# Kernel optimization log

Hardware: AMD Instinct MI355X
Metric: run time of the kernel (lower is better)

## Reference

```python
import jax, jax.numpy as jnp
import numpy as np

B, SX, SY, D = 32, 2048, 2048, 160

def setup_inputs() -> dict:
    key = jax.random.key(0)
    ks = jax.random.split(key, 5)
    s = 1.0 / np.sqrt(D)
    return {
        "x": jax.random.normal(ks[0], (B, SX, D), dtype=jnp.float32),
        "y": jax.random.normal(ks[1], (B, SY, D), dtype=jnp.float32),
        "Wq": jax.random.normal(ks[2], (D, D), dtype=jnp.float32) * s,
        "bq": jnp.zeros((D,), dtype=jnp.float32),
        "Wk": jax.random.normal(ks[3], (D, D), dtype=jnp.float32) * s,
        "bk": jnp.zeros((D,), dtype=jnp.float32),
        "Wv": jax.random.normal(ks[4], (D, D), dtype=jnp.float32) * s,
        "bv": jnp.zeros((D,), dtype=jnp.float32),
    }

def reference(x, y, Wq, bq, Wk, bk, Wv, bv):
    # torch nn.Linear: out = in @ W.T + b, W is [out_dim, in_dim]
    q = jnp.einsum('bxd,ed->bxe', x, Wq) + bq          # [B,SX,D]
    k = jnp.einsum('byd,ed->bye', y, Wk) + bk          # [B,SY,D]
    v = jnp.einsum('byd,ed->bye', y, Wv) + bv          # [B,SY,D]
    scores = jnp.einsum('bxd,byd->bxy', q, k)          # [B,SX,SY] (no scaling in source)
    attn = jax.nn.softmax(scores, axis=-1)
    out = jnp.einsum('bxy,byd->bxd', attn, v)          # dropout is identity at eval
    return out + x                                     # residual
```

## Files before the change

kernel.cpp:

```cpp
#include <hip/hip_runtime.h>

#define LOG2E 1.44269504088896340736f

typedef _Float16 f16;
typedef __attribute__((ext_vector_type(4))) _Float16 f16x4;
typedef __attribute__((ext_vector_type(8))) _Float16 f16x8;
typedef __attribute__((ext_vector_type(4))) float f32x4;
typedef __attribute__((ext_vector_type(8))) unsigned short us8;

#define BB 32
#define SSX 2048
#define SSY 2048
#define DD 160
#define M_TOTAL (BB*SSX)

#define PRS 168
#define VTRS 136
#define RS 168
#define P_RS 72

__device__ __forceinline__ f32x4 mfma16(f16x8 a, f16x8 b, f32x4 c) {
  return __builtin_amdgcn_mfma_f32_16x16x32_f16(a, b, c, 0, 0, 0);
}

__global__ __launch_bounds__(256, 2) void proj_kernel(
    const float* __restrict__ x, const float* __restrict__ y,
    const float* __restrict__ Wq, const float* __restrict__ bq,
    const float* __restrict__ Wk, const float* __restrict__ bk,
    const float* __restrict__ Wv, const float* __restrict__ bv,
    f16* __restrict__ Qw, f16* __restrict__ Kw, f16* __restrict__ Vtw)
{
  __shared__ __align__(16) f16 buf[160*PRS];
  const int t = threadIdx.x;
  const int wave = t >> 6;
  const int lane = t & 63;
  const int quad = lane >> 4;
  const int l16  = lane & 15;
  const int bid  = blockIdx.x;
  const int kind = bid % 3;
  const int tile = bid / 3;
  const int row0 = tile * 128;
  const float* src  = (kind == 0) ? x  : y;
  const float* W    = (kind == 0) ? Wq : (kind == 1 ? Wk : Wv);
  const float* bias = (kind == 0) ? bq : (kind == 1 ? bk : bv);

  for (int i = 0; i < 20; ++i) {
    int idx = t + i*256;
    int r = idx / 40, c4 = idx % 40;
    float4 v = *(const float4*)&src[(size_t)(row0 + r)*DD + c4*4];
    f16x4 h = { (f16)v.x, (f16)v.y, (f16)v.z, (f16)v.w };
    *(f16x4*)&buf[r*PRS + c4*4] = h;
  }
  __syncthreads();
  f16x8 afr0[5], afr1[5];
  #pragma unroll
  for (int ks = 0; ks < 5; ++ks) {
    afr0[ks] = *(const f16x8*)&buf[(wave*32 + l16)*PRS + ks*32 + quad*8];
    afr1[ks] = *(const f16x8*)&buf[(wave*32 + 16 + l16)*PRS + ks*32 + quad*8];
  }
  __syncthreads();

  for (int i = 0; i < 25; ++i) {
    int idx = t + i*256;
    int r = idx / 40, c4 = idx % 40;
    float4 v = *(const float4*)&W[r*160 + c4*4];
    f16x4 h = { (f16)v.x, (f16)v.y, (f16)v.z, (f16)v.w };
    *(f16x4*)&buf[r*PRS + c4*4] = h;
  }
  __syncthreads();

  f32x4 acc0[10], acc1[10];
  #pragma unroll
  for (int nt = 0; nt < 10; ++nt) {
    float bs = bias[nt*16 + l16];
    acc0[nt] = (f32x4){bs,bs,bs,bs};
    acc1[nt] = (f32x4){bs,bs,bs,bs};
    #pragma unroll
    for (int ks = 0; ks < 5; ++ks) {
      f16x8 bfr = *(const f16x8*)&buf[(nt*16 + l16)*PRS + ks*32 + quad*8];
      acc0[nt] = mfma16(afr0[ks], bfr, acc0[nt]);
      acc1[nt] = mfma16(afr1[ks], bfr, acc1[nt]);
    }
  }
  __syncthreads();

  if (kind < 2) {
    f16* dst = (kind == 0) ? Qw : Kw;
    #pragma unroll
    for (int nt = 0; nt < 10; ++nt)
      #pragma unroll
      for (int r = 0; r < 4; ++r) {
        buf[(wave*32 + quad*4 + r)*PRS + nt*16 + l16]      = (f16)acc0[nt][r];
        buf[(wave*32 + 16 + quad*4 + r)*PRS + nt*16 + l16] = (f16)acc1[nt][r];
      }
    __syncthreads();
    for (int i = 0; i < 10; ++i) {
      int idx = t + i*256;
      int r = idx / 20, g = idx % 20;
      *(us8*)&dst[(size_t)(row0 + r)*DD + g*8] = *(const us8*)&buf[r*PRS + g*8];
    }
  } else {
    #pragma unroll
    for (int nt = 0; nt < 10; ++nt)
      #pragma unroll
      for (int r = 0; r < 4; ++r) {
        buf[(nt*16 + l16)*VTRS + wave*32 + quad*4 + r]      = (f16)acc0[nt][r];
        buf[(nt*16 + l16)*VTRS + wave*32 + 16 + quad*4 + r] = (f16)acc1[nt][r];
      }
    __syncthreads();
    const int b  = row0 / SSY;
    const int y0 = row0 % SSY;
    for (int i = 0; i < 10; ++i) {
      int idx = t + i*256;
      int d = idx / 16, yg = idx % 16;
      *(us8*)&Vtw[((size_t)b*DD + d)*SSY + y0 + yg*8] = *(const us8*)&buf[d*VTRS + yg*8];
    }
  }
}


#define LOAD_CHUNK(yb) { \
  const f16* ksrc = Kw + ((size_t)b*SSY + (yb))*DD; \
  const f16* vsrc = Vtw + (size_t)b*DD*SSY + (yb); \
  _Pragma("unroll") \
  for (int i = 0; i < 5; ++i) { \
    int idx = t + i*256; int r = idx/20, c = idx%20; \
    kreg[i] = *(const us8*)&ksrc[(size_t)r*DD + c*8]; \
  } \
  _Pragma("unroll") \
  for (int i = 0; i < 5; ++i) { \
    int idx = t + i*256; int d = idx>>3, g = idx&7; \
    vreg[i] = *(const us8*)&vsrc[(size_t)d*SSY + g*8]; \
  } \
}

#define STORE_CHUNK() { \
  _Pragma("unroll") \
  for (int i = 0; i < 5; ++i) { \
    int idx = t + i*256; int r = idx/20, c = idx%20; \
    *(us8*)&K_lds[r*RS + c*8] = kreg[i]; \
  } \
  _Pragma("unroll") \
  for (int i = 0; i < 5; ++i) { \
    int idx = t + i*256; int d = idx>>3, g = idx&7; \
    *(us8*)&Vt_lds[d*64 + ((g ^ (d & 7)) << 3)] = vreg[i]; \
  } \
}

__global__ __launch_bounds__(256, 2) void flash_kernel(
    const f16* __restrict__ Qw, const f16* __restrict__ Kw, const f16* __restrict__ Vtw,
    const float* __restrict__ x, float* __restrict__ out)
{
  __shared__ __align__(16) f16 K_lds[64*RS];
  __shared__ __align__(16) f16 Vt_lds[176*64];
  __shared__ __align__(16) f16 P_lds[4*32*P_RS];
  const int t = threadIdx.x;
  const int wave = t >> 6;
  const int lane = t & 63;
  const int quad = lane >> 4;
  const int l16  = lane & 15;
  const int bid  = blockIdx.x;
  const int b    = bid >> 4;
  const int x0   = (bid & 15) * 128;

  for (int idx = t; idx < 1024; idx += 256) {
    int d = idx >> 6, yy = idx & 63;
    Vt_lds[(160 + d)*64 + yy] = (d == 0) ? (f16)1.0f : (f16)0.0f;
  }

  f16x8 qfr0[5], qfr1[5];
  #pragma unroll
  for (int h = 0; h < 2; ++h) {
    if (h) __syncthreads();
    const f16* qsrc = Qw + ((size_t)b*SSX + x0 + h*64)*DD;
    for (int i = 0; i < 5; ++i) {
      int idx = t + i*256;
      int r = idx / 20, c = idx % 20;
      *(us8*)&K_lds[r*RS + c*8] = *(const us8*)&qsrc[(size_t)r*DD + c*8];
    }
    __syncthreads();
    if ((wave >> 1) == h) {
      const int base = (wave & 1)*32;
      #pragma unroll
      for (int ks = 0; ks < 5; ++ks) {
        qfr0[ks] = *(const f16x8*)&K_lds[(base + l16)*RS + ks*32 + quad*8];
        qfr1[ks] = *(const f16x8*)&K_lds[(base + 16 + l16)*RS + ks*32 + quad*8];
      }
    }
  }

  f32x4 acc0[11], acc1[11];
  #pragma unroll
  for (int i = 0; i < 11; ++i) { acc0[i] = (f32x4){0.f,0.f,0.f,0.f}; acc1[i] = (f32x4){0.f,0.f,0.f,0.f}; }
  float m0[4], m1[4];
  #pragma unroll
  for (int r = 0; r < 4; ++r) { m0[r] = -1e30f; m1[r] = -1e30f; }

  f16* Pw = &P_lds[wave*32*P_RS];
  us8 kreg[5], vreg[5];

  LOAD_CHUNK(0);
  for (int yc = 0; yc < SSY/64; ++yc) {
    __syncthreads();
    STORE_CHUNK();
    __syncthreads();
    if (yc < SSY/64 - 1) LOAD_CHUNK((yc+1)*64);

    f32x4 S0[4], S1[4];
    #pragma unroll
    for (int nt = 0; nt < 4; ++nt) { S0[nt] = (f32x4){0.f,0.f,0.f,0.f}; S1[nt] = (f32x4){0.f,0.f,0.f,0.f}; }
    #pragma unroll
    for (int nt = 0; nt < 4; ++nt)
      #pragma unroll
      for (int ks = 0; ks < 5; ++ks) {
        f16x8 kfr = *(const f16x8*)&K_lds[(nt*16 + l16)*RS + ks*32 + quad*8];
        S0[nt] = mfma16(qfr0[ks], kfr, S0[nt]);
        S1[nt] = mfma16(qfr1[ks], kfr, S1[nt]);
      }

    float n0[4], n1[4];
    bool changed = false;
    #pragma unroll
    for (int r = 0; r < 4; ++r) {
      float a = fmaxf(fmaxf(S0[0][r], S0[1][r]), fmaxf(S0[2][r], S0[3][r]));
      #pragma unroll
      for (int off = 1; off < 16; off <<= 1) a = fmaxf(a, __shfl_xor(a, off));
      n0[r] = fmaxf(m0[r], a);
      changed = changed || (n0[r] > m0[r]);
      float c = fmaxf(fmaxf(S1[0][r], S1[1][r]), fmaxf(S1[2][r], S1[3][r]));
      #pragma unroll
      for (int off = 1; off < 16; off <<= 1) c = fmaxf(c, __shfl_xor(c, off));
      n1[r] = fmaxf(m1[r], c);
      changed = changed || (n1[r] > m1[r]);
    }
    if (__any(changed)) {
      f32x4 av0, av1;
      #pragma unroll
      for (int r = 0; r < 4; ++r) {
        av0[r] = exp2f((m0[r] - n0[r])*LOG2E); m0[r] = n0[r];
        av1[r] = exp2f((m1[r] - n1[r])*LOG2E); m1[r] = n1[r];
      }
      #pragma unroll
      for (int i = 0; i < 11; ++i) { acc0[i] *= av0; acc1[i] *= av1; }
    }

    #pragma unroll
    for (int r = 0; r < 4; ++r)
      #pragma unroll
      for (int nt = 0; nt < 4; ++nt) {
        Pw[(quad*4 + r)*P_RS + nt*16 + l16]      = (f16)exp2f((S0[nt][r] - m0[r])*LOG2E);
        Pw[(16 + quad*4 + r)*P_RS + nt*16 + l16] = (f16)exp2f((S1[nt][r] - m1[r])*LOG2E);
      }

    #pragma unroll
    for (int k2 = 0; k2 < 2; ++k2) {
      f16x8 p0 = *(const f16x8*)&Pw[l16*P_RS + k2*32 + quad*8];
      f16x8 p1 = *(const f16x8*)&Pw[(16 + l16)*P_RS + k2*32 + quad*8];
      #pragma unroll
      for (int dt = 0; dt < 11; ++dt) {
        f16x8 vfr = *(const f16x8*)&Vt_lds[(dt*16 + l16)*64 + (((k2*4 + quad) ^ (l16 & 7)) << 3)];
        acc0[dt] = mfma16(p0, vfr, acc0[dt]);
        acc1[dt] = mfma16(p1, vfr, acc1[dt]);
      }
    }
  }

  float rl0[4], rl1[4];
  #pragma unroll
  for (int r = 0; r < 4; ++r) {
    rl0[r] = 1.f / __shfl(acc0[10][r], lane & 48);
    rl1[r] = 1.f / __shfl(acc1[10][r], lane & 48);
  }
  const size_t base = ((size_t)b*SSX + x0 + wave*32)*DD;
  #pragma unroll
  for (int dt = 0; dt < 10; ++dt)
    #pragma unroll
    for (int r = 0; r < 4; ++r) {
      size_t o0 = base + (size_t)(quad*4 + r)*DD + dt*16 + l16;
      size_t o1 = base + (size_t)(16 + quad*4 + r)*DD + dt*16 + l16;
      out[o0] = acc0[dt][r]*rl0[r] + x[o0];
      out[o1] = acc1[dt][r]*rl1[r] + x[o1];
    }
}

extern "C" void kernel_launch(void* const* d_in, const int* in_sizes, int n_in,
                              void* d_out, int out_size, void* d_ws, size_t ws_size,
                              hipStream_t stream) {
  const float* x  = (const float*)d_in[0];
  const float* y  = (const float*)d_in[1];
  const float* Wq = (const float*)d_in[2];
  const float* bq = (const float*)d_in[3];
  const float* Wk = (const float*)d_in[4];
  const float* bk = (const float*)d_in[5];
  const float* Wv = (const float*)d_in[6];
  const float* bv = (const float*)d_in[7];

  f16* Qw  = (f16*)d_ws;
  f16* Kw  = Qw + (size_t)M_TOTAL*DD;
  f16* Vtw = Kw + (size_t)M_TOTAL*DD;

  proj_kernel<<<1536, 256, 0, stream>>>(x, y, Wq, bq, Wk, bk, Wv, bv, Qw, Kw, Vtw);
  flash_kernel<<<512, 256, 0, stream>>>(Qw, Kw, Vtw, x, (float*)d_out);
}
```

Baseline: 325.2 us.

## Switch flash attention to 32x32x16 MFMA with register-resident P and lazy rescale

Rewrites the flash attention inner loop to use 32x32x16 MFMA tiles, computing S transposed (K as A operand) so each lane holds one query column. P is then repacked to f16 through cross-half-wave shuffles instead of a round trip through LDS. The row sum is accumulated explicitly rather than through an extra ones column in V, and the output is rescaled only when the max grows by more than a threshold. It also adds s_setprio around the MFMA blocks. These changes remove the P LDS traffic and the extra V tile, at the cost of shuffles and more complex lane mapping.

```diff
diff --git a/kernel.cpp b/kernel.cpp
--- a/kernel.cpp
+++ b/kernel.cpp
@@ -3,9 +3,11 @@
 #define LOG2E 1.44269504088896340736f
 
 typedef _Float16 f16;
+typedef __attribute__((ext_vector_type(2))) _Float16 f16x2;
 typedef __attribute__((ext_vector_type(4))) _Float16 f16x4;
 typedef __attribute__((ext_vector_type(8))) _Float16 f16x8;
 typedef __attribute__((ext_vector_type(4))) float f32x4;
+typedef __attribute__((ext_vector_type(16))) float f32x16;
 typedef __attribute__((ext_vector_type(8))) unsigned short us8;
 
 #define BB 32
@@ -17,10 +19,19 @@
 #define PRS 168
 #define VTRS 136
 #define RS 168
-#define P_RS 72
 
 __device__ __forceinline__ f32x4 mfma16(f16x8 a, f16x8 b, f32x4 c) {
   return __builtin_amdgcn_mfma_f32_16x16x32_f16(a, b, c, 0, 0, 0);
+}
+
+__device__ __forceinline__ f32x16 mfma32(f16x8 a, f16x8 b, f32x16 c) {
+  return __builtin_amdgcn_mfma_f32_32x32x16_f16(a, b, c, 0, 0, 0);
+}
+
+__device__ __forceinline__ unsigned pk2(float a, float b) {
+  union { f16x2 h; unsigned u; } x;
+  x.h = (f16x2){(f16)a, (f16)b};
+  return x.u;
 }
 
 __global__ __launch_bounds__(256, 2) void proj_kernel(
@@ -152,23 +163,17 @@
     const float* __restrict__ x, float* __restrict__ out)
 {
   __shared__ __align__(16) f16 K_lds[64*RS];
-  __shared__ __align__(16) f16 Vt_lds[176*64];
-  __shared__ __align__(16) f16 P_lds[4*32*P_RS];
+  __shared__ __align__(16) f16 Vt_lds[160*64];
   const int t = threadIdx.x;
   const int wave = t >> 6;
   const int lane = t & 63;
-  const int quad = lane >> 4;
-  const int l16  = lane & 15;
+  const int l31  = lane & 31;
+  const int hi   = lane >> 5;
   const int bid  = blockIdx.x;
   const int b    = bid >> 4;
   const int x0   = (bid & 15) * 128;
 
-  for (int idx = t; idx < 1024; idx += 256) {
-    int d = idx >> 6, yy = idx & 63;
-    Vt_lds[(160 + d)*64 + yy] = (d == 0) ? (f16)1.0f : (f16)0.0f;
-  }
-
-  f16x8 qfr0[5], qfr1[5];
+  f16x8 qfr[10];
   #pragma unroll
   for (int h = 0; h < 2; ++h) {
     if (h) __syncthreads();
@@ -182,105 +187,109 @@
     if ((wave >> 1) == h) {
       const int base = (wave & 1)*32;
       #pragma unroll
-      for (int ks = 0; ks < 5; ++ks) {
-        qfr0[ks] = *(const f16x8*)&K_lds[(base + l16)*RS + ks*32 + quad*8];
-        qfr1[ks] = *(const f16x8*)&K_lds[(base + 16 + l16)*RS + ks*32 + quad*8];
-      }
-    }
-  }
-
-  f32x4 acc0[11], acc1[11];
-  #pragma unroll
-  for (int i = 0; i < 11; ++i) { acc0[i] = (f32x4){0.f,0.f,0.f,0.f}; acc1[i] = (f32x4){0.f,0.f,0.f,0.f}; }
-  float m0[4], m1[4];
-  #pragma unroll
-  for (int r = 0; r < 4; ++r) { m0[r] = -1e30f; m1[r] = -1e30f; }
-
-  f16* Pw = &P_lds[wave*32*P_RS];
+      for (int s = 0; s < 10; ++s)
+        qfr[s] = *(const f16x8*)&K_lds[(base + l31)*RS + s*16 + hi*8];
+    }
+  }
+
+  f32x16 acc[5];
+  #pragma unroll
+  for (int i = 0; i < 5; ++i)
+    #pragma unroll
+    for (int r = 0; r < 16; ++r) acc[i][r] = 0.f;
+  float m = -1e30f, l = 0.f;
+
   us8 kreg[5], vreg[5];
-
   LOAD_CHUNK(0);
+
   for (int yc = 0; yc < SSY/64; ++yc) {
     __syncthreads();
     STORE_CHUNK();
     __syncthreads();
     if (yc < SSY/64 - 1) LOAD_CHUNK((yc+1)*64);
 
-    f32x4 S0[4], S1[4];
-    #pragma unroll
-    for (int nt = 0; nt < 4; ++nt) { S0[nt] = (f32x4){0.f,0.f,0.f,0.f}; S1[nt] = (f32x4){0.f,0.f,0.f,0.f}; }
-    #pragma unroll
-    for (int nt = 0; nt < 4; ++nt)
-      #pragma unroll
-      for (int ks = 0; ks < 5; ++ks) {
-        f16x8 kfr = *(const f16x8*)&K_lds[(nt*16 + l16)*RS + ks*32 + quad*8];
-        S0[nt] = mfma16(qfr0[ks], kfr, S0[nt]);
-        S1[nt] = mfma16(qfr1[ks], kfr, S1[nt]);
-      }
-
-    float n0[4], n1[4];
-    bool changed = false;
-    #pragma unroll
-    for (int r = 0; r < 4; ++r) {
-      float a = fmaxf(fmaxf(S0[0][r], S0[1][r]), fmaxf(S0[2][r], S0[3][r]));
-      #pragma unroll
-      for (int off = 1; off < 16; off <<= 1) a = fmaxf(a, __shfl_xor(a, off));
-      n0[r] = fmaxf(m0[r], a);
-      changed = changed || (n0[r] > m0[r]);
-      float c = fmaxf(fmaxf(S1[0][r], S1[1][r]), fmaxf(S1[2][r], S1[3][r]));
-      #pragma unroll
-      for (int off = 1; off < 16; off <<= 1) c = fmaxf(c, __shfl_xor(c, off));
-      n1[r] = fmaxf(m1[r], c);
-      changed = changed || (n1[r] > m1[r]);
-    }
-    if (__any(changed)) {
-      f32x4 av0, av1;
-      #pragma unroll
-      for (int r = 0; r < 4; ++r) {
-        av0[r] = exp2f((m0[r] - n0[r])*LOG2E); m0[r] = n0[r];
-        av1[r] = exp2f((m1[r] - n1[r])*LOG2E); m1[r] = n1[r];
-      }
-      #pragma unroll
-      for (int i = 0; i < 11; ++i) { acc0[i] *= av0; acc1[i] *= av1; }
-    }
-
-    #pragma unroll
-    for (int r = 0; r < 4; ++r)
-      #pragma unroll
-      for (int nt = 0; nt < 4; ++nt) {
-        Pw[(quad*4 + r)*P_RS + nt*16 + l16]      = (f16)exp2f((S0[nt][r] - m0[r])*LOG2E);
-        Pw[(16 + quad*4 + r)*P_RS + nt*16 + l16] = (f16)exp2f((S1[nt][r] - m1[r])*LOG2E);
-      }
-
-    #pragma unroll
-    for (int k2 = 0; k2 < 2; ++k2) {
-      f16x8 p0 = *(const f16x8*)&Pw[l16*P_RS + k2*32 + quad*8];
-      f16x8 p1 = *(const f16x8*)&Pw[(16 + l16)*P_RS + k2*32 + quad*8];
-      #pragma unroll
-      for (int dt = 0; dt < 11; ++dt) {
-        f16x8 vfr = *(const f16x8*)&Vt_lds[(dt*16 + l16)*64 + (((k2*4 + quad) ^ (l16 & 7)) << 3)];
-        acc0[dt] = mfma16(p0, vfr, acc0[dt]);
-        acc1[dt] = mfma16(p1, vfr, acc1[dt]);
-      }
-    }
-  }
-
-  float rl0[4], rl1[4];
-  #pragma unroll
-  for (int r = 0; r < 4; ++r) {
-    rl0[r] = 1.f / __shfl(acc0[10][r], lane & 48);
-    rl1[r] = 1.f / __shfl(acc1[10][r], lane & 48);
-  }
-  const size_t base = ((size_t)b*SSX + x0 + wave*32)*DD;
-  #pragma unroll
-  for (int dt = 0; dt < 10; ++dt)
-    #pragma unroll
-    for (int r = 0; r < 4; ++r) {
-      size_t o0 = base + (size_t)(quad*4 + r)*DD + dt*16 + l16;
-      size_t o1 = base + (size_t)(16 + quad*4 + r)*DD + dt*16 + l16;
-      out[o0] = acc0[dt][r]*rl0[r] + x[o0];
-      out[o1] = acc1[dt][r]*rl1[r] + x[o1];
-    }
+    f32x16 S0, S1;
+    #pragma unroll
+    for (int r = 0; r < 16; ++r) { S0[r] = 0.f; S1[r] = 0.f; }
+    __builtin_amdgcn_s_setprio(1);
+    #pragma unroll
+    for (int s = 0; s < 10; ++s) {
+      f16x8 k0 = *(const f16x8*)&K_lds[l31*RS + s*16 + hi*8];
+      f16x8 k1 = *(const f16x8*)&K_lds[(32 + l31)*RS + s*16 + hi*8];
+      S0 = mfma32(k0, qfr[s], S0);
+      S1 = mfma32(k1, qfr[s], S1);
+    }
+    __builtin_amdgcn_s_setprio(0);
+
+    float pmax = S0[0];
+    #pragma unroll
+    for (int r = 1; r < 16; ++r) pmax = fmaxf(pmax, S0[r]);
+    #pragma unroll
+    for (int r = 0; r < 16; ++r) pmax = fmaxf(pmax, S1[r]);
+    pmax = fmaxf(pmax, __shfl_xor(pmax, 32));
+
+    if (__any(pmax > m + 8.f)) {
+      float n  = fmaxf(m, pmax);
+      float sc = exp2f((m - n)*LOG2E);
+      m = n; l *= sc;
+      #pragma unroll
+      for (int r = 0; r < 16; ++r) {
+        float scq = __shfl(sc, (r&3) + 8*(r>>2) + 4*hi);
+        #pragma unroll
+        for (int dt = 0; dt < 5; ++dt) acc[dt][r] *= scq;
+      }
+    }
+
+    float lsum = 0.f;
+    #pragma unroll
+    for (int r = 0; r < 16; ++r) { S0[r] = exp2f((S0[r] - m)*LOG2E); lsum += S0[r]; }
+    #pragma unroll
+    for (int r = 0; r < 16; ++r) { S1[r] = exp2f((S1[r] - m)*LOG2E); lsum += S1[r]; }
+    lsum += __shfl_xor(lsum, 32);
+    l += lsum;
+
+    #pragma unroll
+    for (int c = 0; c < 4; ++c) {
+      const int bo = (c & 1)*8;
+      unsigned L0, L1, H0, H1;
+      if (c < 2) {
+        L0 = pk2(S0[bo+0], S0[bo+1]); L1 = pk2(S0[bo+2], S0[bo+3]);
+        H0 = pk2(S0[bo+4], S0[bo+5]); H1 = pk2(S0[bo+6], S0[bo+7]);
+      } else {
+        L0 = pk2(S1[bo+0], S1[bo+1]); L1 = pk2(S1[bo+2], S1[bo+3]);
+        H0 = pk2(S1[bo+4], S1[bo+5]); H1 = pk2(S1[bo+6], S1[bo+7]);
+      }
+      unsigned sd0 = hi ? L0 : H0;
+      unsigned sd1 = hi ? L1 : H1;
+      unsigned rc0 = (unsigned)__shfl_xor((int)sd0, 32);
+      unsigned rc1 = (unsigned)__shfl_xor((int)sd1, 32);
+      union { unsigned u[4]; f16x8 h; } pw;
+      pw.u[0] = hi ? rc0 : L0;
+      pw.u[1] = hi ? rc1 : L1;
+      pw.u[2] = hi ? H0 : rc0;
+      pw.u[3] = hi ? H1 : rc1;
+      __builtin_amdgcn_s_setprio(1);
+      #pragma unroll
+      for (int dt = 0; dt < 5; ++dt) {
+        int row = dt*32 + l31;
+        f16x8 vf = *(const f16x8*)&Vt_lds[row*64 + (((c*2 + hi) ^ (row & 7)) << 3)];
+        acc[dt] = mfma32(pw.h, vf, acc[dt]);
+      }
+      __builtin_amdgcn_s_setprio(0);
+    }
+  }
+
+  #pragma unroll
+  for (int r = 0; r < 16; ++r) {
+    int qr = (r&3) + 8*(r>>2) + 4*hi;
+    float rl = 1.f / __shfl(l, qr);
+    size_t rowoff = ((size_t)b*SSX + x0 + wave*32 + qr)*DD + l31;
+    #pragma unroll
+    for (int dt = 0; dt < 5; ++dt) {
+      size_t o = rowoff + (size_t)dt*32;
+      out[o] = acc[dt][r]*rl + x[o];
+    }
+  }
 }
 
 extern "C" void kernel_launch(void* const* d_in, const int* in_sizes, int n_in,
```

Result: faster. 299.4 us (-7.9%).
